# Kernel optimization log

Hardware: AMD Instinct MI355X
Metric: run time of the kernel (lower is better)

## Reference

```python
import jax, jax.numpy as jnp
import numpy as np

EMB_DIM = 1024
NUM_HEAD = 16
HEAD_DIM = EMB_DIM // NUM_HEAD
B, S = 2, 2048


def setup_inputs() -> dict:
    key = jax.random.key(0)
    ks = jax.random.split(key, 10)
    scale = 1.0 / np.sqrt(EMB_DIM)
    x = jax.random.normal(ks[0], (B, S, EMB_DIM), dtype=jnp.float32)
    # causal mask: 1 = keep, 0 = masked out (torch masked_fill(mask == 0, -inf))
    mask = jnp.tril(jnp.ones((S, S), dtype=jnp.int32))[None, None, :, :]
    def lin(kw, kb):
        W = jax.random.uniform(kw, (EMB_DIM, EMB_DIM), jnp.float32, -scale, scale)
        b = jax.random.uniform(kb, (EMB_DIM,), jnp.float32, -scale, scale)
        return W, b
    Wq, bq = lin(ks[1], ks[2])
    Wk, bk = lin(ks[3], ks[4])
    Wv, bv = lin(ks[5], ks[6])
    Wo, bo = lin(ks[7], ks[8])
    return {"x": x, "mask": mask, "Wq": Wq, "bq": bq, "Wk": Wk, "bk": bk,
            "Wv": Wv, "bv": bv, "Wo": Wo, "bo": bo}


def reference(x, mask, Wq, bq, Wk, bk, Wv, bv, Wo, bo):
    Bsz, Sq, _ = x.shape
    # projections; torch Linear: y = x @ W^T + b
    def proj(W, b):
        y = jnp.einsum('bse,fe->bsf', x, W) + b
        return y.reshape(Bsz, Sq, NUM_HEAD, HEAD_DIM).transpose(0, 2, 1, 3)  # [B,H,S,D]
    q = proj(Wq, bq)
    k = proj(Wk, bk)
    v = proj(Wv, bv)
    scaling = jnp.asarray(HEAD_DIM ** 0.5, x.dtype)
    scores = jnp.einsum('bhqd,bhkd->bhqk', q, k) / scaling  # [B,H,S,S]
    scores = jnp.where(mask == 0, -jnp.inf, scores)
    attn = jax.nn.softmax(scores, axis=-1)
    out = jnp.einsum('bhqk,bhkd->bhqd', attn, v)
    out = out.transpose(0, 2, 1, 3).reshape(Bsz, Sq, EMB_DIM)
    return jnp.einsum('bse,fe->bsf', out, Wo) + bo
```

## Files before the change

### kernel.cpp

```cpp
#include <hip/hip_runtime.h>

typedef unsigned short u16;
typedef __attribute__((ext_vector_type(8))) __bf16 bf16x8;
typedef __attribute__((ext_vector_type(8))) short  short8;
typedef __attribute__((ext_vector_type(4))) short  short4v;
typedef __attribute__((ext_vector_type(4))) float  floatx4;
typedef __attribute__((ext_vector_type(4))) int    intx4;
typedef __attribute__((ext_vector_type(2))) int    intx2;

constexpr int Bc = 2, Sc = 2048, Ec = 1024, Hc = 16, Dc = 64;
constexpr int Mc = Bc * Sc;

#define QSCALE  0.18033688011112042f

__device__ __forceinline__ u16 f2b(float f) {
  union { float f; unsigned u; } c; c.f = f;
  unsigned u = c.u;
  return (u16)((u + 0x7fffu + ((u >> 16) & 1u)) >> 16);
}
__device__ __forceinline__ short8 ld8(const u16* p) { return *(const short8*)p; }

__device__ __forceinline__ int cvt_pk(float lo, float hi) {
  int r;
  asm("v_cvt_pk_bf16_f32 %0, %1, %2" : "=v"(r) : "v"(lo), "v"(hi));
  return r;
}

__device__ __forceinline__ floatx4 mfma16(short8 a, short8 b, floatx4 c) {
  return __builtin_amdgcn_mfma_f32_16x16x32_bf16(
      __builtin_bit_cast(bf16x8, a), __builtin_bit_cast(bf16x8, b), c, 0, 0, 0);
}

__device__ __forceinline__ void async16(const u16* g, u16* l) {
  __builtin_amdgcn_global_load_lds(
      (const __attribute__((address_space(1))) void*)g,
      (__attribute__((address_space(3))) void*)l, 16, 0, 0);
}

__global__ __launch_bounds__(256) void cvt_kernel(
    const float* __restrict__ x,  const float* __restrict__ Wq,
    const float* __restrict__ Wk, const float* __restrict__ Wv,
    const float* __restrict__ Wo, u16* __restrict__ dst) {
  const size_t i = ((size_t)blockIdx.x * 256 + threadIdx.x) * 4;
  const int seg = (int)(i >> 20);
  const float* src;
  size_t off;
  if (seg < 4)       { src = x;  off = i; }
  else if (seg == 4) { src = Wq; off = i - ((size_t)4 << 20); }
  else if (seg == 5) { src = Wk; off = i - ((size_t)5 << 20); }
  else if (seg == 6) { src = Wv; off = i - ((size_t)6 << 20); }
  else               { src = Wo; off = i - ((size_t)7 << 20); }
  floatx4 v = *(const floatx4*)(src + off);
  intx2 o;
  o[0] = cvt_pk(v[0], v[1]);
  o[1] = cvt_pk(v[2], v[3]);
  *(intx2*)(dst + i) = o;
}

__device__ __forceinline__ void gemm64x128(
    const u16* __restrict__ A, const u16* __restrict__ B, int K,
    int m0, int n0, u16* As, u16* Bs, floatx4 acc[2][4]) {
  const int t = threadIdx.x;
  const int w = t >> 6, lane = t & 63;
  const int wm = w & 1, wn = w >> 1;
  const int quad = lane >> 4, l16 = lane & 15;
  const int r = t >> 2;
  const int c = (t & 3) * 8;

#pragma unroll
  for (int i = 0; i < 2; ++i)
#pragma unroll
    for (int j = 0; j < 4; ++j) acc[i][j] = 0.f;

  for (int k0 = 0; k0 < K; k0 += 32) {
    async16(A + (size_t)(m0 + r) * K + k0 + c, As + w * 512);
#pragma unroll
    for (int jj = 0; jj < 2; ++jj)
      async16(B + (size_t)(n0 + jj * 64 + r) * K + k0 + c, Bs + jj * 2048 + w * 512);
    __syncthreads();
    short8 af[2], bfr[4];
#pragma unroll
    for (int i = 0; i < 2; ++i)
      af[i]  = *(const short8*)(As + (wm * 32 + i * 16 + l16) * 32 + quad * 8);
#pragma unroll
    for (int j = 0; j < 4; ++j)
      bfr[j] = *(const short8*)(Bs + (wn * 64 + j * 16 + l16) * 32 + quad * 8);
#pragma unroll
    for (int i = 0; i < 2; ++i)
#pragma unroll
      for (int j = 0; j < 4; ++j)
        acc[i][j] = mfma16(af[i], bfr[j], acc[i][j]);
    __syncthreads();
  }
}

__global__ __launch_bounds__(256, 6) void qkv_mm(
    const u16* __restrict__ xb, const u16* __restrict__ Wb,
    const float* __restrict__ bq, const float* __restrict__ bk,
    const float* __restrict__ bv,
    u16* __restrict__ Q, u16* __restrict__ K_, u16* __restrict__ Vt) {
  __shared__ __align__(16) u16 As[2048], Bs[4096];
  const int z = blockIdx.z;
  const u16* W = Wb + ((size_t)z << 20);
  const float* bias = (z == 0) ? bq : (z == 1) ? bk : bv;
  const int m0 = blockIdx.y * 64, n0 = blockIdx.x * 128;

  floatx4 acc[2][4];
  gemm64x128(xb, W, Ec, m0, n0, As, Bs, acc);

  const int t = threadIdx.x, w = t >> 6, lane = t & 63;
  const int wm = w & 1, wn = w >> 1, quad = lane >> 4, l16 = lane & 15;
#pragma unroll
  for (int i = 0; i < 2; ++i)
#pragma unroll
    for (int j = 0; j < 4; ++j)
#pragma unroll
      for (int rr = 0; rr < 4; ++rr) {
        const int row = m0 + wm * 32 + i * 16 + quad * 4 + rr;
        const int col = n0 + wn * 64 + j * 16 + l16;
        float v = acc[i][j][rr] + bias[col];
        if (z == 0) v *= QSCALE;
        const int bb = row >> 11, s = row & (Sc - 1);
        const int h = col >> 6, d = col & (Dc - 1), bh = bb * Hc + h;
        if (z < 2) ((z == 0) ? Q : K_)[((size_t)bh * Sc + s) * Dc + d] = f2b(v);
        else {
          const int sp = (s & ~31) | ((s & 12) << 1) | ((s & 16) >> 2) | (s & 3);
          Vt[((size_t)bh * Dc + d) * Sc + sp] = f2b(v);
        }
      }
}

__global__ __launch_bounds__(256, 6) void proj_mm(
    const u16* __restrict__ O, const u16* __restrict__ Wob,
    const float* __restrict__ bias, float* __restrict__ out) {
  __shared__ __align__(16) u16 As[2048], Bs[4096];
  const int m0 = blockIdx.y * 64, n0 = blockIdx.x * 128;

  floatx4 acc[2][4];
  gemm64x128(O, Wob, Ec, m0, n0, As, Bs, acc);

  const int t = threadIdx.x, w = t >> 6, lane = t & 63;
  const int wm = w & 1, wn = w >> 1, quad = lane >> 4, l16 = lane & 15;
#pragma unroll
  for (int i = 0; i < 2; ++i)
#pragma unroll
    for (int j = 0; j < 4; ++j)
#pragma unroll
      for (int rr = 0; rr < 4; ++rr) {
        const int row = m0 + wm * 32 + i * 16 + quad * 4 + rr;
        const int col = n0 + wn * 64 + j * 16 + l16;
        out[(size_t)row * Ec + col] = acc[i][j][rr] + bias[col];
      }
}

__global__ __launch_bounds__(256, 4) void attn_kernel(
    const u16* __restrict__ Q, const u16* __restrict__ K,
    const u16* __restrict__ Vt, u16* __restrict__ O) {
  const int v  = blockIdx.x & 31, g8 = blockIdx.x >> 5, kk = blockIdx.y;
  const int q1 = (kk & 2) ? ((v + 8) & 31) : v;
  const int qt = (kk & 1) ? (31 - q1) : q1;
  const int q0 = qt * 64;
  const int bh = kk * 8 + g8;
  const int bb = bh >> 4, h = bh & 15;

  const u16* Qh = Q  + (size_t)bh * Sc * Dc;
  const u16* Kh = K  + (size_t)bh * Sc * Dc;
  const u16* Vh = Vt + (size_t)bh * Dc * Sc;

  const int t = threadIdx.x;
  const int w = t >> 6, lane = t & 63;
  const int quad = lane >> 4, l16 = lane & 15;

  __shared__ __align__(16) u16 Ks[8192];
  __shared__ __align__(16) u16 Vs[8192];

  const int sr = w * 8 + (lane >> 3);
  const int sb = (lane & 7) ^ (lane >> 3);
  const int swz = l16 & 7;

  const u16* qrow_p = Qh + (size_t)(q0 + w * 16 + l16) * Dc;
  const short8 aq0 = ld8(qrow_p + quad * 8);
  const short8 aq1 = ld8(qrow_p + 32 + quad * 8);

  float   lrow = 0.f;
  floatx4 oacc[4];
#pragma unroll
  for (int dt = 0; dt < 4; ++dt) oacc[dt] = 0.f;

  for (int kt = 0; kt <= q0; kt += 128) {
#pragma unroll
    for (int st = 0; st < 2; ++st)
#pragma unroll
      for (int it = 0; it < 2; ++it) {
        const int r = it * 32 + sr;
        async16(Kh + (size_t)(kt + st * 64 + r) * Dc + sb * 8,
                Ks + st * 4096 + it * 2048 + w * 512);
        async16(Vh + (size_t)r * Sc + kt + st * 64 + sb * 8,
                Vs + st * 4096 + it * 2048 + w * 512);
      }
    __syncthreads();

    floatx4 sacc[8];
#pragma unroll
    for (int g = 0; g < 8; ++g) sacc[g] = 0.f;
#pragma unroll
    for (int ks = 0; ks < 2; ++ks) {
      const short8 bq = ks ? aq1 : aq0;
#pragma unroll
      for (int g = 0; g < 8; ++g) {
        const short8 a = *(const short8*)(
            Ks + (g >> 2) * 4096 + ((g & 3) * 16 + l16) * 64 +
            (((ks * 4 + quad) ^ swz) * 8));
        sacc[g] = mfma16(a, bq, sacc[g]);
      }
    }

    const bool diag = (kt + 128 > q0);
    const int thr = q0 + w * 16 + l16 - kt - 4 * quad;
#pragma unroll
    for (int g = 0; g < 8; ++g)
#pragma unroll
      for (int r = 0; r < 4; ++r) {
        float pv = exp2f(sacc[g][r]);
        if (diag && (16 * g + r > thr)) pv = 0.f;
        lrow += pv;
        sacc[g][r] = pv;
      }

    short8 pa[4];
#pragma unroll
    for (int c = 0; c < 4; ++c) {
      intx4 wd;
      wd[0] = cvt_pk(sacc[2 * c][0],     sacc[2 * c][1]);
      wd[1] = cvt_pk(sacc[2 * c][2],     sacc[2 * c][3]);
      wd[2] = cvt_pk(sacc[2 * c + 1][0], sacc[2 * c + 1][1]);
      wd[3] = cvt_pk(sacc[2 * c + 1][2], sacc[2 * c + 1][3]);
      pa[c] = __builtin_bit_cast(short8, wd);
    }

#pragma unroll
    for (int c = 0; c < 4; ++c) {
      const int st = c >> 1, kcl = c & 1;
#pragma unroll
      for (int dt = 0; dt < 4; ++dt) {
        const short8 b = *(const short8*)(
            Vs + st * 4096 + (dt * 16 + l16) * 64 +
            (((kcl * 4 + quad) ^ swz) * 8));
        oacc[dt] = mfma16(pa[c], b, oacc[dt]);
      }
    }
    __syncthreads();
  }

  lrow += __shfl_xor(lrow, 16);
  lrow += __shfl_xor(lrow, 32);
  float rs[4];
#pragma unroll
  for (int r = 0; r < 4; ++r)
    rs[r] = 1.f / __shfl(lrow, quad * 4 + r, 16);

#pragma unroll
  for (int dt = 0; dt < 4; ++dt) {
#pragma unroll
    for (int r = 0; r < 4; ++r) {
      const int qrow = q0 + w * 16 + quad * 4 + r;
      O[((size_t)(bb * Sc + qrow)) * Ec + h * Dc + dt * 16 + l16] =
          f2b(oacc[dt][r] * rs[r]);
    }
  }
}

extern "C" void kernel_launch(void* const* d_in, const int* in_sizes, int n_in,
                              void* d_out, int out_size, void* d_ws, size_t ws_size,
                              hipStream_t stream) {
  const float* x  = (const float*)d_in[0];
  const float* Wq = (const float*)d_in[2];
  const float* bq = (const float*)d_in[3];
  const float* Wk = (const float*)d_in[4];
  const float* bk = (const float*)d_in[5];
  const float* Wv = (const float*)d_in[6];
  const float* bv = (const float*)d_in[7];
  const float* Wo = (const float*)d_in[8];
  const float* bo = (const float*)d_in[9];

  const size_t MiE = (size_t)Mc * Ec;
  u16* Q  = (u16*)d_ws;
  u16* K  = Q  + MiE;
  u16* Vt = K  + MiE;
  u16* O  = Vt + MiE;
  u16* xb = O  + MiE;
  u16* Wb = xb + MiE;
  u16* Wob = Wb + ((size_t)3 << 20);

  cvt_kernel<<<8192, 256, 0, stream>>>(x, Wq, Wk, Wv, Wo, xb);
  qkv_mm<<<dim3(Ec / 128, Mc / 64, 3), 256, 0, stream>>>(
      xb, Wb, bq, bk, bv, Q, K, Vt);
  attn_kernel<<<dim3(256, 4), 256, 0, stream>>>(Q, K, Vt, O);
  proj_mm<<<dim3(Ec / 128, Mc / 64), 256, 0, stream>>>(O, Wob, bo, (float*)d_out);
}
```

Baseline: 215.1 us.

## Double-buffer GEMM LDS tiles with async prefetch and XOR-swizzle layout

```diff
diff --git a/kernel.cpp b/kernel.cpp
--- a/kernel.cpp
+++ b/kernel.cpp
@@ -65,32 +65,58 @@
   const int wm = w & 1, wn = w >> 1;
   const int quad = lane >> 4, l16 = lane & 15;
   const int r = t >> 2;
-  const int c = (t & 3) * 8;
+  const int c = ((t & 3) ^ ((t >> 3) & 3)) * 8;
+  const int rs = (quad ^ ((l16 >> 1) & 3)) * 8;
+
+  const u16* ap  = A + (size_t)(m0 + r) * K + c;
+  const u16* bp0 = B + (size_t)(n0 + r) * K + c;
+  const u16* bp1 = B + (size_t)(n0 + 64 + r) * K + c;
+  u16* const al  = As + w * 512;
+  u16* const bl0 = Bs + w * 512;
+  u16* const bl1 = Bs + 2048 + w * 512;
 
 #pragma unroll
   for (int i = 0; i < 2; ++i)
 #pragma unroll
     for (int j = 0; j < 4; ++j) acc[i][j] = 0.f;
 
+  async16(ap,  al);
+  async16(bp0, bl0);
+  async16(bp1, bl1);
+
+  int cur = 0;
   for (int k0 = 0; k0 < K; k0 += 32) {
-    async16(A + (size_t)(m0 + r) * K + k0 + c, As + w * 512);
-#pragma unroll
-    for (int jj = 0; jj < 2; ++jj)
-      async16(B + (size_t)(n0 + jj * 64 + r) * K + k0 + c, Bs + jj * 2048 + w * 512);
-    __syncthreads();
+    if (k0 + 32 < K) {
+      const int nb = cur ^ 1;
+      async16(ap  + k0 + 32, al  + nb * 2048);
+      async16(bp0 + k0 + 32, bl0 + nb * 4096);
+      async16(bp1 + k0 + 32, bl1 + nb * 4096);
+      __builtin_amdgcn_sched_barrier(0);
+      asm volatile("s_waitcnt vmcnt(3)");
+    } else {
+      asm volatile("s_waitcnt vmcnt(0)");
+    }
+    __builtin_amdgcn_s_barrier();
+    __builtin_amdgcn_sched_barrier(0);
+
     short8 af[2], bfr[4];
 #pragma unroll
     for (int i = 0; i < 2; ++i)
-      af[i]  = *(const short8*)(As + (wm * 32 + i * 16 + l16) * 32 + quad * 8);
+      af[i]  = *(const short8*)(As + cur * 2048 +
+                                (wm * 32 + i * 16 + l16) * 32 + rs);
 #pragma unroll
     for (int j = 0; j < 4; ++j)
-      bfr[j] = *(const short8*)(Bs + (wn * 64 + j * 16 + l16) * 32 + quad * 8);
+      bfr[j] = *(const short8*)(Bs + cur * 4096 +
+                                (wn * 64 + j * 16 + l16) * 32 + rs);
 #pragma unroll
     for (int i = 0; i < 2; ++i)
 #pragma unroll
       for (int j = 0; j < 4; ++j)
         acc[i][j] = mfma16(af[i], bfr[j], acc[i][j]);
-    __syncthreads();
+
+    __builtin_amdgcn_sched_barrier(0);
+    __builtin_amdgcn_s_barrier();
+    cur ^= 1;
   }
 }
 
@@ -99,7 +125,7 @@
     const float* __restrict__ bq, const float* __restrict__ bk,
     const float* __restrict__ bv,
     u16* __restrict__ Q, u16* __restrict__ K_, u16* __restrict__ Vt) {
-  __shared__ __align__(16) u16 As[2048], Bs[4096];
+  __shared__ __align__(16) u16 As[4096], Bs[8192];
   const int z = blockIdx.z;
   const u16* W = Wb + ((size_t)z << 20);
   const float* bias = (z == 0) ? bq : (z == 1) ? bk : bv;
@@ -133,7 +159,7 @@
 __global__ __launch_bounds__(256, 6) void proj_mm(
     const u16* __restrict__ O, const u16* __restrict__ Wob,
     const float* __restrict__ bias, float* __restrict__ out) {
-  __shared__ __align__(16) u16 As[2048], Bs[4096];
+  __shared__ __align__(16) u16 As[4096], Bs[8192];
   const int m0 = blockIdx.y * 64, n0 = blockIdx.x * 128;
 
   floatx4 acc[2][4];
```

Measured after the change: 212.2 us. Within noise of the previous version (-1.3%).
